# Kernel tuning notes

Hardware: AMD Instinct MI355X
Metric: run time of the kernel (lower is better)

## Reference

```python
import jax, jax.numpy as jnp
import numpy as np
import math

WINDOW_SIZE = 4
NUM_HEADS = 4


def _l2norm(x, eps=1e-12):
    # matches torch F.normalize(dim=-1): x / max(||x||, eps)
    n = jnp.linalg.norm(x, axis=-1, keepdims=True)
    return x / jnp.maximum(n, eps)


def setup_inputs() -> dict:
    key = jax.random.key(0)
    kq, kk, kv, km = jax.random.split(key, 4)
    Q, B, C = 262144, 1, 128
    L = 262144  # H*W = 512*512
    N = WINDOW_SIZE * WINDOW_SIZE  # 16
    q = jax.random.normal(kq, (Q, B, C), dtype=jnp.float32)
    k = jax.random.normal(kk, (L, B, C), dtype=jnp.float32)
    v = jax.random.normal(kv, (L, B, C), dtype=jnp.float32)
    mask = 0.1 * jax.random.normal(km, (1, Q, N), dtype=jnp.float32)  # nW=1 additive mask
    logit_scale = jnp.log(10.0) * jnp.ones((NUM_HEADS, 1, 1), dtype=jnp.float32)
    return {"q": q, "k": k, "v": v, "H": 512, "W": 512, "mask": mask,
            "logit_scale": logit_scale}


def reference(q, k, v, H, W, mask, logit_scale):
    ws = WINDOW_SIZE
    nh = NUM_HEADS
    L, B, C = k.shape
    Q = q.shape[0]
    hd = C // nh
    N = ws * ws

    q = q.reshape(B, Q, C)
    k = k.reshape(B, H, W, C)
    v = v.reshape(B, H, W, C)

    # window partition: (B,H,W,C) -> (B*nWin, ws*ws, C)
    def part(x):
        x = x.reshape(B, H // ws, ws, W // ws, ws, C)
        x = x.transpose(0, 1, 3, 2, 4, 5)
        return x.reshape(-1, N, C)

    k = part(k)
    v = part(v)
    B_ = k.shape[0]

    # heads: q (B, nh, Q, hd); k,v (B_, nh, N, hd)
    q = q.reshape(B, Q, nh, hd).transpose(0, 2, 1, 3)
    k = k.reshape(B_, N, nh, hd).transpose(0, 2, 1, 3)
    v = v.reshape(B_, N, nh, hd).transpose(0, 2, 1, 3)

    # mean-pool k/v across all windows (dim 0); requires B == 1
    k = jnp.mean(k, axis=0).reshape(B, nh, N, hd)
    v = jnp.mean(v, axis=0).reshape(B, nh, N, hd)

    # cosine-similarity attention with clamped learned temperature
    attn = jnp.einsum('bhqd,bhkd->bhqk', _l2norm(q), _l2norm(k))
    scale = jnp.exp(jnp.minimum(logit_scale, math.log(1.0 / 0.01)))  # (nh,1,1)
    attn = attn * scale[None]

    # additive mask with nW = mask.shape[0] = 1: broadcast over heads
    attn = attn + mask[:, None, :, :]

    attn = jax.nn.softmax(attn, axis=-1)
    x = jnp.einsum('bhqk,bhkd->bhqd', attn, v)  # (B, nh, Q, hd)
    x = x.transpose(0, 2, 1, 3).reshape(B, Q, nh * hd)
    return x.reshape(Q, B, C)
```

## Files before the change

kernel.cpp:

```cpp
#include <hip/hip_runtime.h>


template <int CTRL>
__device__ __forceinline__ float dppf(float x) {
    return __int_as_float(
        __builtin_amdgcn_update_dpp(0, __float_as_int(x), CTRL, 0xF, 0xF, true));
}
#define DPP_XOR1 0xB1
#define DPP_XOR2 0x4E
#define DPP_MIR8 0x141

template <int IMM>
__device__ __forceinline__ float swzf(float x) {
    return __int_as_float(__builtin_amdgcn_ds_swizzle(__float_as_int(x), IMM));
}

#define ADD4(A, B) { A.x += B.x; A.y += B.y; A.z += B.z; A.w += B.w; }

#define GLOAD4NT(dst, base, vo) \
    asm volatile("global_load_dwordx4 %0, %1, %2 nt" \
                 : "=v"(dst) : "v"(vo), "s"(base) : "memory")
#define WAITV(n) asm volatile("s_waitcnt vmcnt(" #n ")" ::: "memory")
#define SBAR() __builtin_amdgcn_sched_barrier(0)

__device__ __forceinline__ void gload_lds16(const float4* g, void* l) {
    __builtin_amdgcn_global_load_lds(
        (const __attribute__((address_space(1))) unsigned int*)(const void*)g,
        (__attribute__((address_space(3))) unsigned int*)l, 16, 0, 0);
}

__global__ __launch_bounds__(256, 1) void k_reduce_p1(const float4* __restrict__ k4,
                                                      const float4* __restrict__ v4,
                                                      float4* __restrict__ p4) {
    __shared__ float4 red[256];
    const int t = threadIdx.x;
    const int b = blockIdx.x;
    const bool isv = (b >= 512);
    const int bb = b & 511;
    const float4* __restrict__ src = isv ? v4 : k4;
    const unsigned vbase = (unsigned)(bb * 256 + t) * 16u;

    float4 a0, a1, a2, a3, a4, a5, a6, a7;
    float4 b0, b1, b2, b3, b4, b5, b6, b7;
    float4 z = make_float4(0.f, 0.f, 0.f, 0.f);
    float4 acc0 = z, acc1 = z, acc2 = z, acc3 = z;

#define OFF(g, i) (vbase + (unsigned)(((g) * 8 + (i)) * 2097152u))
#define ISSUE(G, g) \
    GLOAD4NT(G##0, src, OFF(g, 0)); GLOAD4NT(G##1, src, OFF(g, 1)); \
    GLOAD4NT(G##2, src, OFF(g, 2)); GLOAD4NT(G##3, src, OFF(g, 3)); \
    GLOAD4NT(G##4, src, OFF(g, 4)); GLOAD4NT(G##5, src, OFF(g, 5)); \
    GLOAD4NT(G##6, src, OFF(g, 6)); GLOAD4NT(G##7, src, OFF(g, 7))
#define CONSUME_A() \
    ADD4(acc0, a0); ADD4(acc1, a1); ADD4(acc2, a2); ADD4(acc3, a3); \
    ADD4(acc0, a4); ADD4(acc1, a5); ADD4(acc2, a6); ADD4(acc3, a7)
#define CONSUME_B() \
    ADD4(acc0, b0); ADD4(acc1, b1); ADD4(acc2, b2); ADD4(acc3, b3); \
    ADD4(acc0, b4); ADD4(acc1, b5); ADD4(acc2, b6); ADD4(acc3, b7)

    ISSUE(a, 0);  ISSUE(b, 1);
    WAITV(8); SBAR(); CONSUME_A(); ISSUE(a, 2);
    WAITV(8); SBAR(); CONSUME_B(); ISSUE(b, 3);
    WAITV(8); SBAR(); CONSUME_A(); ISSUE(a, 4);
    WAITV(8); SBAR(); CONSUME_B(); ISSUE(b, 5);
    WAITV(8); SBAR(); CONSUME_A(); ISSUE(a, 6);
    WAITV(8); SBAR(); CONSUME_B(); ISSUE(b, 7);
    WAITV(8); SBAR(); CONSUME_A();
    WAITV(0); SBAR(); CONSUME_B();

    ADD4(acc0, acc1);
    ADD4(acc2, acc3);
    ADD4(acc0, acc2);
    red[t] = acc0;
    __syncthreads();

    if (t < 128) {
        float4 s = red[t];
        const float4 p = red[t + 128];
        ADD4(s, p);
        p4[(isv ? 65536 : 0) + bb * 128 + t] = s;
    }
}

__global__ __launch_bounds__(256) void k_finish(const float4* __restrict__ p4,
                                                const float* __restrict__ logit_scale,
                                                float4* __restrict__ k2f4,
                                                float4* __restrict__ v2f4) {
    __shared__ float4 lsum[256];
    const int b = blockIdx.x;
    const int srcv = b >> 4;
    const int rc = (b >> 2) & 3;
    const int cc = b & 3;
    const int n = rc * 4 + cc;
    const int t = threadIdx.x;
    const int w0 = t >> 5;
    const int q = t & 31;

    const float4* base = p4 + srcv * 65536 + cc * 32 + q;
    float4 s = make_float4(0.f, 0.f, 0.f, 0.f);
#pragma unroll
    for (int b1 = 0; b1 < 2; ++b1) {
#pragma unroll
        for (int j = 0; j < 8; ++j) {
            const int bb = b1 * 256 + rc * 64 + w0 * 8 + j;
            const float4 x = base[bb * 128];
            ADD4(s, x);
        }
    }
    lsum[t] = s;
    __syncthreads();

    if (t < 32) {
        float4 m = lsum[t];
#pragma unroll
        for (int w = 1; w < 8; ++w) {
            const float4 x = lsum[w * 32 + t];
            ADD4(m, x);
        }
        const float inv = 1.0f / 16384.0f;
        m.x *= inv; m.y *= inv; m.z *= inv; m.w *= inv;

        const int h = t >> 3;
        const int dq = t & 7;
        if (srcv == 0) {
            float ss = m.x * m.x + m.y * m.y + m.z * m.z + m.w * m.w;
            ss += dppf<DPP_XOR1>(ss);
            ss += dppf<DPP_XOR2>(ss);
            ss += dppf<DPP_MIR8>(ss);
            const float sc = __expf(fminf(logit_scale[h], 4.6051702f));
            const float f = sc / fmaxf(sqrtf(ss), 1e-12f);
            k2f4[h * 128 + n * 8 + dq] = make_float4(m.x * f, m.y * f, m.z * f, m.w * f);
        } else {
            v2f4[h * 128 + n * 8 + dq] = m;
        }
    }
}

__global__ __launch_bounds__(256) void k_reduce_atomic(const float4* __restrict__ k4,
                                                       const float4* __restrict__ v4,
                                                       float* __restrict__ ksum,
                                                       float* __restrict__ vsum) {
    __shared__ float4 stage[2048];
    __shared__ float4 redE[256];
    __shared__ float4 redO[256];
    const int t = threadIdx.x;
    const int b = blockIdx.x;
    const bool isv = (b >= 1024);
    const int bb = b & 1023;
    const float4* __restrict__ src = isv ? v4 : k4;
    float* __restrict__ dst = isv ? vsum : ksum;

    const int wv = t >> 6;
    const int ln = t & 63;
    const long gstart = (long)bb * 8192 + wv * 2048;
    const float4* gsrc = src + gstart + ln;
    char* lbase = (char*)stage + wv * 8192;

#pragma unroll
    for (int j = 0; j < 4; ++j)
        gload_lds16(gsrc + j * 64, lbase + j * 1024);

    float4 z = make_float4(0.f, 0.f, 0.f, 0.f);
    float4 accE = z, accO = z;

#pragma unroll
    for (int c = 0; c < 8; ++c) {
        if (c < 7) {
            const int p1 = (c + 1) & 1;
#pragma unroll
            for (int j = 0; j < 4; ++j)
                gload_lds16(gsrc + (c + 1) * 256 + j * 64,
                            lbase + p1 * 4096 + j * 1024);
            asm volatile("s_waitcnt vmcnt(4)" ::: "memory");
        } else {
            asm volatile("s_waitcnt vmcnt(0)" ::: "memory");
        }
        __builtin_amdgcn_sched_barrier(0);
        const int p = c & 1;
        const float4* lf = (const float4*)(lbase + p * 4096) + ln;
        const float4 x0 = lf[0];
        const float4 x1 = lf[64];
        const float4 x2 = lf[128];
        const float4 x3 = lf[192];
        ADD4(accE, x0); ADD4(accO, x1); ADD4(accE, x2); ADD4(accO, x3);
    }

    redE[wv * 64 + ln] = accE;
    redO[wv * 64 + ln] = accO;
    __syncthreads();

    if (t < 128) {
        const int n0 = t >> 5;
        const int c4 = t & 31;
        const float4* arr = (n0 < 2) ? redE : redO;
        const int base = (n0 & 1) * 32 + c4;
        float4 s = arr[base];
        const float4 s1 = arr[base + 64];
        const float4 s2 = arr[base + 128];
        const float4 s3 = arr[base + 192];
        ADD4(s, s1); ADD4(s, s2); ADD4(s, s3);
        const int n = ((bb >> 1) & 3) * 4 + n0;
        const int c = c4 * 4;
        atomicAdd(&dst[n * 128 + c + 0], s.x);
        atomicAdd(&dst[n * 128 + c + 1], s.y);
        atomicAdd(&dst[n * 128 + c + 2], s.z);
        atomicAdd(&dst[n * 128 + c + 3], s.w);
    }
}

__global__ __launch_bounds__(256) void k_prep(const float* __restrict__ ksum,
                                              const float* __restrict__ vsum,
                                              const float* __restrict__ logit_scale,
                                              float* __restrict__ k2,
                                              float* __restrict__ v2) {
    __shared__ float mk[2048], mv[2048], fac[64];
    const int t = threadIdx.x;
    const float inv = 1.0f / 16384.0f;
    for (int w = t; w < 2048; w += 256) {
        mk[w] = ksum[w] * inv;
        mv[w] = vsum[w] * inv;
    }
    __syncthreads();
    if (t < 64) {
        const int h = t >> 4, n = t & 15;
        float ss = 0.f;
#pragma unroll
        for (int d = 0; d < 32; ++d) {
            float x = mk[n * 128 + h * 32 + d];
            ss += x * x;
        }
        const float nrm = sqrtf(ss);
        const float sc = __expf(fminf(logit_scale[h], 4.6051702f));
        fac[t] = sc / fmaxf(nrm, 1e-12f);
    }
    __syncthreads();
    for (int w = t; w < 2048; w += 256) {
        const int h = w >> 9;
        const int n = (w & 511) >> 5;
        const int d = w & 31;
        const float f = fac[h * 16 + n];
        k2[w] = mk[n * 128 + h * 32 + d] * f;
        v2[w] = mv[n * 128 + h * 32 + d];
    }
}

__global__ __launch_bounds__(256, 2) void k_attn(const float4* __restrict__ q4,
                                                 const float2* __restrict__ mask2,
                                                 const float4* __restrict__ k2f4,
                                                 const float4* __restrict__ v2f4,
                                                 float4* __restrict__ out4) {
    const int t = threadIdx.x;
    const int isub = t >> 5;
    const int l5 = t & 31;
    const int h = l5 >> 3;
    const int g = l5 & 7;

    float4 kreg[16], vreg[16];
#pragma unroll
    for (int n = 0; n < 16; ++n) {
        kreg[n] = k2f4[h * 128 + n * 8 + g];
        vreg[n] = v2f4[h * 128 + n * 8 + g];
    }

    const bool b2 = (g & 4) != 0;
    const bool b1 = (g & 2) != 0;
    const bool b0 = (g & 1) != 0;

    auto process = [&](const float4 qv, const float2 mw) -> float4 {
        float ss = qv.x * qv.x + qv.y * qv.y + qv.z * qv.z + qv.w * qv.w;
        ss += dppf<DPP_XOR1>(ss);
        ss += dppf<DPP_XOR2>(ss);
        ss += dppf<DPP_MIR8>(ss);
        const float rn = rsqrtf(fmaxf(ss, 1e-24f));
        const float qx = qv.x * rn, qy = qv.y * rn, qz = qv.z * rn, qw = qv.w * rn;

        float part[16];
#pragma unroll
        for (int n = 0; n < 16; ++n)
            part[n] = qx * kreg[n].x + qy * kreg[n].y + qz * kreg[n].z + qw * kreg[n].w;

        float r8[8];
#pragma unroll
        for (int j = 0; j < 8; ++j) {
            const float snd = b2 ? part[j] : part[j + 8];
            const float kp  = b2 ? part[j + 8] : part[j];
            r8[j] = kp + dppf<DPP_MIR8>(snd);
        }
        float r4[4];
#pragma unroll
        for (int j = 0; j < 4; ++j) {
            const float snd = b1 ? r8[j] : r8[j + 4];
            const float kp  = b1 ? r8[j + 4] : r8[j];
            r4[j] = kp + dppf<DPP_XOR2>(snd);
        }
        float s0, s1;
        {
            const float sndA = b0 ? r4[0] : r4[2];
            const float kpA  = b0 ? r4[2] : r4[0];
            s0 = kpA + dppf<DPP_XOR1>(sndA);
            const float sndB = b0 ? r4[1] : r4[3];
            const float kpB  = b0 ? r4[3] : r4[1];
            s1 = kpB + dppf<DPP_XOR1>(sndB);
        }

        const float e0 = __expf(s0 + mw.x);
        const float e1 = __expf(s1 + mw.y);

        float ds = e0 + e1;
        ds += dppf<DPP_XOR1>(ds);
        ds += dppf<DPP_XOR2>(ds);
        ds += dppf<DPP_MIR8>(ds);
        const float rden = 1.0f / ds;

        float pf[16];
        pf[0]  = swzf<(0 << 5) | 0x18>(e0);
        pf[1]  = swzf<(0 << 5) | 0x18>(e1);
        pf[2]  = swzf<(1 << 5) | 0x18>(e0);
        pf[3]  = swzf<(1 << 5) | 0x18>(e1);
        pf[4]  = swzf<(2 << 5) | 0x18>(e0);
        pf[5]  = swzf<(2 << 5) | 0x18>(e1);
        pf[6]  = swzf<(3 << 5) | 0x18>(e0);
        pf[7]  = swzf<(3 << 5) | 0x18>(e1);
        pf[8]  = swzf<(4 << 5) | 0x18>(e0);
        pf[9]  = swzf<(4 << 5) | 0x18>(e1);
        pf[10] = swzf<(5 << 5) | 0x18>(e0);
        pf[11] = swzf<(5 << 5) | 0x18>(e1);
        pf[12] = swzf<(6 << 5) | 0x18>(e0);
        pf[13] = swzf<(6 << 5) | 0x18>(e1);
        pf[14] = swzf<(7 << 5) | 0x18>(e0);
        pf[15] = swzf<(7 << 5) | 0x18>(e1);

        float ox = 0.f, oy = 0.f, oz = 0.f, ow = 0.f;
#pragma unroll
        for (int n = 0; n < 16; ++n) {
            ox += pf[n] * vreg[n].x;
            oy += pf[n] * vreg[n].y;
            oz += pf[n] * vreg[n].z;
            ow += pf[n] * vreg[n].w;
        }
        return make_float4(ox * rden, oy * rden, oz * rden, ow * rden);
    };

    int i = blockIdx.x * 128 + isub;
    float4 qA = q4[i * 32 + h * 8 + g];
    float4 qB = q4[(i + 8) * 32 + h * 8 + g];
    float2 mA = mask2[i * 8 + g];
    float2 mB = mask2[(i + 8) * 8 + g];

#pragma unroll 1
    for (int iter = 0; iter < 8; ++iter) {
        const int ip = (iter < 7) ? (i + 16) : i;
        const float4 qA_n = q4[ip * 32 + h * 8 + g];
        const float4 qB_n = q4[(ip + 8) * 32 + h * 8 + g];
        const float2 mA_n = mask2[ip * 8 + g];
        const float2 mB_n = mask2[(ip + 8) * 8 + g];

        const float4 oA = process(qA, mA);
        const float4 oB = process(qB, mB);
        out4[i * 32 + h * 8 + g] = oA;
        out4[(i + 8) * 32 + h * 8 + g] = oB;

        i += 16;
        qA = qA_n; qB = qB_n; mA = mA_n; mB = mB_n;
    }
}

extern "C" void kernel_launch(void* const* d_in, const int* in_sizes, int n_in,
                              void* d_out, int out_size, void* d_ws, size_t ws_size,
                              hipStream_t stream) {
    (void)in_sizes; (void)n_in; (void)out_size;
    const float* q = (const float*)d_in[0];
    const float* k = (const float*)d_in[1];
    const float* v = (const float*)d_in[2];
    const float* mask = (const float*)d_in[5];
    const float* ls = (const float*)d_in[6];

    float* ws = (float*)d_ws;
    float* ksum = ws;
    float* vsum = ws + 2048;
    float* k2 = ws + 4096;
    float* v2 = ws + 6144;
    float* part = ws + 8192;

    const size_t needed = (size_t)8192 * 4 + (size_t)131072 * 16;
    if (ws_size >= needed) {
        k_reduce_p1<<<1024, 256, 0, stream>>>((const float4*)k, (const float4*)v,
                                              (float4*)part);
        k_finish<<<32, 256, 0, stream>>>((const float4*)part, ls,
                                         (float4*)k2, (float4*)v2);
    } else {
        hipMemsetAsync(ws, 0, 4096 * sizeof(float), stream);
        k_reduce_atomic<<<2048, 256, 0, stream>>>((const float4*)k, (const float4*)v,
                                                  ksum, vsum);
        k_prep<<<1, 256, 0, stream>>>(ksum, vsum, ls, k2, v2);
    }
    k_attn<<<2048, 256, 0, stream>>>((const float4*)q, (const float2*)mask,
                                     (const float4*)k2, (const float4*)v2,
                                     (float4*)d_out);
}
```

Measured before the change: 119.2 us.

## Compute attention with bf16 MFMA tiles and pre-laid-out bf16 K/V operands

Replaces the scalar attention kernel with one that runs both the QK^T and PV products for 16 queries per wave on 16x16x32 bf16 MFMA instructions. The finish kernel now writes normalized K and mean V in bf16, already swizzled into the MFMA operand layout, with zero padding for the unused K dimension. The aim is to cut ALU and shuffle work in the attention kernel, which is mostly bound by streaming q, mask and output. In exchange, q, the softmax probabilities and V are rounded to bf16, which lowers accuracy, and the PV step spends half of each MFMA on padding.

```diff
diff --git a/kernel.cpp b/kernel.cpp
--- a/kernel.cpp
+++ b/kernel.cpp
@@ -1,5 +1,9 @@
 #include <hip/hip_runtime.h>
 
+
+typedef __attribute__((ext_vector_type(8))) short bf16x8;
+typedef __attribute__((ext_vector_type(4))) float f32x4;
+union F4S8 { float4 f; bf16x8 s; };
 
 template <int CTRL>
 __device__ __forceinline__ float dppf(float x) {
@@ -27,6 +31,16 @@
     __builtin_amdgcn_global_load_lds(
         (const __attribute__((address_space(1))) unsigned int*)(const void*)g,
         (__attribute__((address_space(3))) unsigned int*)l, 16, 0, 0);
+}
+
+__device__ __forceinline__ unsigned short bf16rne(float x) {
+    unsigned u = __float_as_uint(x);
+    return (unsigned short)((u + 0x7fffu + ((u >> 16) & 1u)) >> 16);
+}
+__device__ __forceinline__ unsigned cvtpk_bf16(float lo, float hi) {
+    unsigned r;
+    asm("v_cvt_pk_bf16_f32 %0, %1, %2" : "=v"(r) : "v"(lo), "v"(hi));
+    return r;
 }
 
 __global__ __launch_bounds__(256, 1) void k_reduce_p1(const float4* __restrict__ k4,
@@ -84,9 +98,11 @@
 
 __global__ __launch_bounds__(256) void k_finish(const float4* __restrict__ p4,
                                                 const float* __restrict__ logit_scale,
-                                                float4* __restrict__ k2f4,
-                                                float4* __restrict__ v2f4) {
+                                                float4* __restrict__ k2bf4,
+                                                float* __restrict__ v2b_base) {
     __shared__ float4 lsum[256];
+    __shared__ unsigned short kb16[128];
+    __shared__ float vb32[128];
     const int b = blockIdx.x;
     const int srcv = b >> 4;
     const int rc = (b >> 2) & 3;
@@ -120,18 +136,131 @@
         const float inv = 1.0f / 16384.0f;
         m.x *= inv; m.y *= inv; m.z *= inv; m.w *= inv;
 
-        const int h = t >> 3;
-        const int dq = t & 7;
         if (srcv == 0) {
+            const int h = t >> 3;
             float ss = m.x * m.x + m.y * m.y + m.z * m.z + m.w * m.w;
             ss += dppf<DPP_XOR1>(ss);
             ss += dppf<DPP_XOR2>(ss);
             ss += dppf<DPP_MIR8>(ss);
             const float sc = __expf(fminf(logit_scale[h], 4.6051702f));
             const float f = sc / fmaxf(sqrtf(ss), 1e-12f);
-            k2f4[h * 128 + n * 8 + dq] = make_float4(m.x * f, m.y * f, m.z * f, m.w * f);
+            kb16[4 * t + 0] = bf16rne(m.x * f);
+            kb16[4 * t + 1] = bf16rne(m.y * f);
+            kb16[4 * t + 2] = bf16rne(m.z * f);
+            kb16[4 * t + 3] = bf16rne(m.w * f);
         } else {
-            v2f4[h * 128 + n * 8 + dq] = m;
+            vb32[4 * t + 0] = m.x;
+            vb32[4 * t + 1] = m.y;
+            vb32[4 * t + 2] = m.z;
+            vb32[4 * t + 3] = m.w;
+        }
+    }
+    __syncthreads();
+
+    if (srcv == 0) {
+        if (t < 16) {
+            const int h = t >> 2, lg = t & 3;
+            const uint4* kb4 = (const uint4*)kb16;
+            const uint4 rec = kb4[h * 4 + lg];
+            k2bf4[h * 64 + n + lg * 16] = make_float4(
+                __uint_as_float(rec.x), __uint_as_float(rec.y),
+                __uint_as_float(rec.z), __uint_as_float(rec.w));
+        }
+    } else {
+        unsigned short* v2u16 = (unsigned short*)v2b_base;
+        unsigned* v2u32 = (unsigned*)v2b_base;
+        if (t < 128) {
+            const int h = t >> 5, hf = (t >> 4) & 1, d = t & 15;
+            const int l = (n >> 3) * 16 + d;
+            const int j = n & 7;
+            v2u16[((h * 2 + hf) * 64 + l) * 8 + j] = bf16rne(vb32[h * 32 + hf * 16 + d]);
+        }
+        if (t < 64) {
+            const int gi = n * 64 + t;
+            const int fg = gi >> 7;
+            const int rem = gi & 127;
+            const int l2 = 32 + (rem >> 2);
+            const int c = rem & 3;
+            v2u32[(fg * 64 + l2) * 4 + c] = 0u;
+        }
+    }
+}
+
+__global__ __launch_bounds__(256) void k_attn_mfma(const float4* __restrict__ q4,
+                                                   const float4* __restrict__ mask4,
+                                                   const float4* __restrict__ k2b,
+                                                   const float4* __restrict__ v2b,
+                                                   float* __restrict__ outp) {
+    const int tid = threadIdx.x;
+    const int l = tid & 63, wv = tid >> 6;
+    const int gw = blockIdx.x * 4 + wv;
+    const int ql = l & 15, g4 = l >> 4;
+    const int qq = gw * 16 + ql;
+
+    F4S8 kb[4];
+    F4S8 vb[8];
+#pragma unroll
+    for (int h = 0; h < 4; ++h) kb[h].f = k2b[h * 64 + l];
+#pragma unroll
+    for (int i = 0; i < 8; ++i) vb[i].f = v2b[i * 64 + l];
+
+    float4 qa[4], qb[4];
+#pragma unroll
+    for (int h = 0; h < 4; ++h) {
+        qa[h] = q4[qq * 32 + h * 8 + g4 * 2];
+        qb[h] = q4[qq * 32 + h * 8 + g4 * 2 + 1];
+    }
+    const float4 mk = mask4[qq * 4 + g4];
+
+    const f32x4 z4 = {0.f, 0.f, 0.f, 0.f};
+    const int src0 = ql + g4 * 32;
+    const int src1 = src0 + 16;
+
+#pragma unroll
+    for (int h = 0; h < 4; ++h) {
+        float ss = qa[h].x * qa[h].x + qa[h].y * qa[h].y + qa[h].z * qa[h].z + qa[h].w * qa[h].w
+                 + qb[h].x * qb[h].x + qb[h].y * qb[h].y + qb[h].z * qb[h].z + qb[h].w * qb[h].w;
+        ss += __shfl_xor(ss, 16, 64);
+        ss += __shfl_xor(ss, 32, 64);
+        const float rn = rsqrtf(fmaxf(ss, 1e-24f));
+
+        F4S8 af;
+        af.f = make_float4(
+            __uint_as_float(cvtpk_bf16(qa[h].x * rn, qa[h].y * rn)),
+            __uint_as_float(cvtpk_bf16(qa[h].z * rn, qa[h].w * rn)),
+            __uint_as_float(cvtpk_bf16(qb[h].x * rn, qb[h].y * rn)),
+            __uint_as_float(cvtpk_bf16(qb[h].z * rn, qb[h].w * rn)));
+
+        f32x4 st = __builtin_amdgcn_mfma_f32_16x16x32_bf16(kb[h].s, af.s, z4, 0, 0, 0);
+
+        const float e0 = __expf(st[0] + mk.x);
+        const float e1 = __expf(st[1] + mk.y);
+        const float e2 = __expf(st[2] + mk.z);
+        const float e3 = __expf(st[3] + mk.w);
+        float ds = (e0 + e1) + (e2 + e3);
+        ds += __shfl_xor(ds, 16, 64);
+        ds += __shfl_xor(ds, 32, 64);
+        const float rden = 1.0f / ds;
+
+        const unsigned a01 = cvtpk_bf16(e0 * rden, e1 * rden);
+        const unsigned a23 = cvtpk_bf16(e2 * rden, e3 * rden);
+
+        const unsigned u0 = (unsigned)__shfl((int)a01, src0 & 63, 64);
+        const unsigned u1 = (unsigned)__shfl((int)a23, src0 & 63, 64);
+        const unsigned u2 = (unsigned)__shfl((int)a01, src1 & 63, 64);
+        const unsigned u3 = (unsigned)__shfl((int)a23, src1 & 63, 64);
+        F4S8 pa;
+        pa.f = make_float4(__uint_as_float(u0), __uint_as_float(u1),
+                           __uint_as_float(u2), __uint_as_float(u3));
+
+        f32x4 olo = __builtin_amdgcn_mfma_f32_16x16x32_bf16(pa.s, vb[h * 2 + 0].s, z4, 0, 0, 0);
+        f32x4 ohi = __builtin_amdgcn_mfma_f32_16x16x32_bf16(pa.s, vb[h * 2 + 1].s, z4, 0, 0, 0);
+
+        float* ob = outp + (size_t)(gw * 16 + g4 * 4) * 128 + h * 32 + ql;
+#pragma unroll
+        for (int r = 0; r < 4; ++r) {
+            __builtin_nontemporal_store(olo[r], ob + r * 128);
+            __builtin_nontemporal_store(ohi[r], ob + r * 128 + 16);
         }
     }
 }
@@ -378,6 +507,8 @@
     float* ws = (float*)d_ws;
     float* ksum = ws;
     float* vsum = ws + 2048;
+    float* k2b = ws + 4096;
+    float* v2b = ws + 5120;
     float* k2 = ws + 4096;
     float* v2 = ws + 6144;
     float* part = ws + 8192;
@@ -387,14 +518,17 @@
         k_reduce_p1<<<1024, 256, 0, stream>>>((const float4*)k, (const float4*)v,
                                               (float4*)part);
         k_finish<<<32, 256, 0, stream>>>((const float4*)part, ls,
-                                         (float4*)k2, (float4*)v2);
+                                         (float4*)k2b, v2b);
+        k_attn_mfma<<<4096, 256, 0, stream>>>((const float4*)q, (const float4*)mask,
+                                              (const float4*)k2b, (const float4*)v2b,
+                                              (float*)d_out);
     } else {
         hipMemsetAsync(ws, 0, 4096 * sizeof(float), stream);
         k_reduce_atomic<<<2048, 256, 0, stream>>>((const float4*)k, (const float4*)v,
                                                   ksum, vsum);
         k_prep<<<1, 256, 0, stream>>>(ksum, vsum, ls, k2, v2);
-    }
-    k_attn<<<2048, 256, 0, stream>>>((const float4*)q, (const float2*)mask,
-                                     (const float4*)k2, (const float4*)v2,
-                                     (float4*)d_out);
-}
+        k_attn<<<2048, 256, 0, stream>>>((const float4*)q, (const float2*)mask,
+                                         (const float4*)k2, (const float4*)v2,
+                                         (float4*)d_out);
+    }
+}
```

New measurement: 99.26 us, median of 2. 1.2x faster.
